# Kernel tuning notes

Hardware: AMD Instinct MI355X
Metric: run time of the kernel (lower is better)

Reference implementation:

```python
import jax, jax.numpy as jnp
import numpy as np

B, P, ENC = 32, 196, 2048   # batch, num_pixels, encoder_dim
A, D, E = 512, 512, 512     # attention_dim, decoder_dim, embed_dim
V, L = 32000, 40            # vocab_size, caption length
T = L - 1                   # max decode steps (static)


def setup_inputs() -> dict:
    key = jax.random.key(0)
    ks = jax.random.split(key, 20)
    u = lambda k, shape, s=0.05: jax.random.uniform(k, shape, jnp.float32, -s, s)
    caplens = jax.random.randint(ks[2], (B,), 5, L + 1).at[0].set(L)
    return {
        "encoder_out": jax.random.normal(ks[0], (B, P, ENC), jnp.float32),
        "encoded_captions": jax.random.randint(ks[1], (B, L), 0, V),
        "caption_lengths": caplens,
        "embedding": u(ks[3], (V, E), 0.1),
        "W_enc": u(ks[4], (ENC, A)), "b_enc": jnp.zeros((A,), jnp.float32),
        "W_dec": u(ks[5], (D, A)),   "b_dec": jnp.zeros((A,), jnp.float32),
        "w_att": u(ks[6], (A, 1)),   "b_att": jnp.zeros((1,), jnp.float32),
        "W_ih": u(ks[7], (E + ENC, 4 * D)), "b_ih": jnp.zeros((4 * D,), jnp.float32),
        "W_hh": u(ks[8], (D, 4 * D)),       "b_hh": jnp.zeros((4 * D,), jnp.float32),
        "W_h": u(ks[9], (ENC, D)),  "b_h": jnp.zeros((D,), jnp.float32),
        "W_c": u(ks[10], (ENC, D)), "b_c": jnp.zeros((D,), jnp.float32),
        "W_fb": u(ks[11], (D, ENC)), "b_fb": jnp.zeros((ENC,), jnp.float32),
        "W_fc": u(ks[12], (D, V), 0.1), "b_fc": jnp.zeros((V,), jnp.float32),
    }


def reference(encoder_out, encoded_captions, caption_lengths, embedding,
              W_enc, b_enc, W_dec, b_dec, w_att, b_att,
              W_ih, b_ih, W_hh, b_hh, W_h, b_h, W_c, b_c,
              W_fb, b_fb, W_fc, b_fc):
    dec_len = caption_lengths - 1                       # [B]
    embs = embedding[encoded_captions]                  # [B, L, E]
    avg = encoder_out.mean(axis=1)                      # [B, ENC]
    h0 = avg @ W_h + b_h                                # [B, D]
    c0 = avg @ W_c + b_c
    enc_att = encoder_out @ W_enc + b_enc               # [B, P, A] (loop-invariant)

    xs = (jnp.transpose(embs[:, :T], (1, 0, 2)), jnp.arange(T))

    def step(carry, xt):
        h, c = carry
        emb_t, t = xt                                   # [B, E], scalar
        active = dec_len > t                            # [B] bool
        dec = h @ W_dec + b_dec                         # [B, A]
        e = (jax.nn.relu(enc_att + dec[:, None, :]) @ w_att)[..., 0] + b_att[0]  # [B, P]
        alpha = jax.nn.softmax(e, axis=1)               # [B, P]
        awe = jnp.einsum('bp,bpd->bd', alpha, encoder_out)
        gate = jax.nn.sigmoid(h @ W_fb + b_fb)          # [B, ENC]
        awe = gate * awe
        x = jnp.concatenate([emb_t, awe], axis=-1)      # [B, E+ENC]
        g = x @ W_ih + b_ih + h @ W_hh + b_hh           # [B, 4D]
        i_, f_, g_, o_ = jnp.split(g, 4, axis=-1)
        c_new = jax.nn.sigmoid(f_) * c + jax.nn.sigmoid(i_) * jnp.tanh(g_)
        h_new = jax.nn.sigmoid(o_) * jnp.tanh(c_new)
        preds = h_new @ W_fc + b_fc                     # [B, V]
        m = active[:, None].astype(h.dtype)
        h = jnp.where(active[:, None], h_new, h)        # only active rows advance
        c = jnp.where(active[:, None], c_new, c)
        return (h, c), (preds * m, alpha * m)

    (_, _), (preds, alphas) = jax.lax.scan(step, (h0, c0), xs)
    predictions = jnp.transpose(preds, (1, 0, 2))       # [B, T, V]
    alphas = jnp.transpose(alphas, (1, 0, 2))           # [B, T, P]
    return predictions, alphas
```

## Files before the change

### kernel.cpp

```cpp
#include <hip/hip_runtime.h>
#include <math.h>

#define NB 32
#define NP 196
#define ENC 2048
#define VOC 32000
#define LCAP 40
#define TS 39

typedef unsigned int uint_t;
typedef unsigned short ushort_t;

__device__ __forceinline__ float sigm(float x) { return 1.f / (1.f + expf(-x)); }

__device__ __forceinline__ ushort_t f2bf(float f) {
  uint_t u = __float_as_uint(f);
  u = (u + 0x7FFFu + ((u >> 16) & 1u)) >> 16;
  return (ushort_t)u;
}
__device__ __forceinline__ float bf2f(ushort_t s) { return __uint_as_float(((uint_t)s) << 16); }

typedef __attribute__((ext_vector_type(8))) short bf8v;
typedef __attribute__((ext_vector_type(16))) float f16v;
typedef __attribute__((ext_vector_type(4))) float f4v;

__device__ __forceinline__ f16v MFMA(bf8v a, bf8v b, f16v c) {
  return __builtin_amdgcn_mfma_f32_32x32x16_bf16(a, b, c, 0, 0, 0);
}

__device__ __forceinline__ void mfma_pipe_frag(
    const ushort_t* __restrict__ pa_h, const ushort_t* __restrict__ pa_l,
    const ushort_t* __restrict__ pb_h, const ushort_t* __restrict__ pb_l,
    int nquad, f16v& acc)
{
  bf8v ah0 = *(const bf8v*)(pa_h +    0), al0 = *(const bf8v*)(pa_l +    0);
  bf8v bh0 = *(const bf8v*)(pb_h +    0), bl0 = *(const bf8v*)(pb_l +    0);
  bf8v ah1 = *(const bf8v*)(pa_h +  512), al1 = *(const bf8v*)(pa_l +  512);
  bf8v bh1 = *(const bf8v*)(pb_h +  512), bl1 = *(const bf8v*)(pb_l +  512);
  bf8v ah2 = *(const bf8v*)(pa_h + 1024), al2 = *(const bf8v*)(pa_l + 1024);
  bf8v bh2 = *(const bf8v*)(pb_h + 1024), bl2 = *(const bf8v*)(pb_l + 1024);
  bf8v ah3 = *(const bf8v*)(pa_h + 1536), al3 = *(const bf8v*)(pa_l + 1536);
  bf8v bh3 = *(const bf8v*)(pb_h + 1536), bl3 = *(const bf8v*)(pb_l + 1536);
  for (int q = 0; q < nquad; ++q) {
    const size_t nk = (size_t)(q + 1) * 2048;
    const bool more = (q + 1 < nquad);
    acc = MFMA(ah0, bh0, acc); acc = MFMA(ah0, bl0, acc); acc = MFMA(al0, bh0, acc);
    if (more) {
      ah0 = *(const bf8v*)(pa_h + nk +    0); al0 = *(const bf8v*)(pa_l + nk +    0);
      bh0 = *(const bf8v*)(pb_h + nk +    0); bl0 = *(const bf8v*)(pb_l + nk +    0);
    }
    acc = MFMA(ah1, bh1, acc); acc = MFMA(ah1, bl1, acc); acc = MFMA(al1, bh1, acc);
    if (more) {
      ah1 = *(const bf8v*)(pa_h + nk +  512); al1 = *(const bf8v*)(pa_l + nk +  512);
      bh1 = *(const bf8v*)(pb_h + nk +  512); bl1 = *(const bf8v*)(pb_l + nk +  512);
    }
    acc = MFMA(ah2, bh2, acc); acc = MFMA(ah2, bl2, acc); acc = MFMA(al2, bh2, acc);
    if (more) {
      ah2 = *(const bf8v*)(pa_h + nk + 1024); al2 = *(const bf8v*)(pa_l + nk + 1024);
      bh2 = *(const bf8v*)(pb_h + nk + 1024); bl2 = *(const bf8v*)(pb_l + nk + 1024);
    }
    acc = MFMA(ah3, bh3, acc); acc = MFMA(ah3, bl3, acc); acc = MFMA(al3, bh3, acc);
    if (more) {
      ah3 = *(const bf8v*)(pa_h + nk + 1536); al3 = *(const bf8v*)(pa_l + nk + 1536);
      bh3 = *(const bf8v*)(pb_h + nk + 1536); bl3 = *(const bf8v*)(pb_l + nk + 1536);
    }
  }
}

__device__ __forceinline__ void mfma_pipe_fragAH(
    const ushort_t* __restrict__ pa_h,
    const ushort_t* __restrict__ pb_h, const ushort_t* __restrict__ pb_l,
    int nquad, f16v& acc)
{
  bf8v ah0 = *(const bf8v*)(pa_h +    0);
  bf8v bh0 = *(const bf8v*)(pb_h +    0), bl0 = *(const bf8v*)(pb_l +    0);
  bf8v ah1 = *(const bf8v*)(pa_h +  512);
  bf8v bh1 = *(const bf8v*)(pb_h +  512), bl1 = *(const bf8v*)(pb_l +  512);
  bf8v ah2 = *(const bf8v*)(pa_h + 1024);
  bf8v bh2 = *(const bf8v*)(pb_h + 1024), bl2 = *(const bf8v*)(pb_l + 1024);
  bf8v ah3 = *(const bf8v*)(pa_h + 1536);
  bf8v bh3 = *(const bf8v*)(pb_h + 1536), bl3 = *(const bf8v*)(pb_l + 1536);
  for (int q = 0; q < nquad; ++q) {
    const size_t nk = (size_t)(q + 1) * 2048;
    const bool more = (q + 1 < nquad);
    acc = MFMA(ah0, bh0, acc); acc = MFMA(ah0, bl0, acc);
    if (more) {
      ah0 = *(const bf8v*)(pa_h + nk +    0);
      bh0 = *(const bf8v*)(pb_h + nk +    0); bl0 = *(const bf8v*)(pb_l + nk +    0);
    }
    acc = MFMA(ah1, bh1, acc); acc = MFMA(ah1, bl1, acc);
    if (more) {
      ah1 = *(const bf8v*)(pa_h + nk +  512);
      bh1 = *(const bf8v*)(pb_h + nk +  512); bl1 = *(const bf8v*)(pb_l + nk +  512);
    }
    acc = MFMA(ah2, bh2, acc); acc = MFMA(ah2, bl2, acc);
    if (more) {
      ah2 = *(const bf8v*)(pa_h + nk + 1024);
      bh2 = *(const bf8v*)(pb_h + nk + 1024); bl2 = *(const bf8v*)(pb_l + nk + 1024);
    }
    acc = MFMA(ah3, bh3, acc); acc = MFMA(ah3, bl3, acc);
    if (more) {
      ah3 = *(const bf8v*)(pa_h + nk + 1536);
      bh3 = *(const bf8v*)(pb_h + nk + 1536); bl3 = *(const bf8v*)(pb_l + nk + 1536);
    }
  }
}

__device__ __forceinline__ void mfma_pipe_fragHH(
    const ushort_t* __restrict__ pa_h,
    const ushort_t* __restrict__ pb_h, int nquad, f16v& acc)
{
  bf8v ah0 = *(const bf8v*)(pa_h +    0);
  bf8v bh0 = *(const bf8v*)(pb_h +    0);
  bf8v ah1 = *(const bf8v*)(pa_h +  512);
  bf8v bh1 = *(const bf8v*)(pb_h +  512);
  bf8v ah2 = *(const bf8v*)(pa_h + 1024);
  bf8v bh2 = *(const bf8v*)(pb_h + 1024);
  bf8v ah3 = *(const bf8v*)(pa_h + 1536);
  bf8v bh3 = *(const bf8v*)(pb_h + 1536);
  for (int q = 0; q < nquad; ++q) {
    const size_t nk = (size_t)(q + 1) * 2048;
    const bool more = (q + 1 < nquad);
    acc = MFMA(ah0, bh0, acc);
    if (more) { ah0 = *(const bf8v*)(pa_h + nk +    0); bh0 = *(const bf8v*)(pb_h + nk +    0); }
    acc = MFMA(ah1, bh1, acc);
    if (more) { ah1 = *(const bf8v*)(pa_h + nk +  512); bh1 = *(const bf8v*)(pb_h + nk +  512); }
    acc = MFMA(ah2, bh2, acc);
    if (more) { ah2 = *(const bf8v*)(pa_h + nk + 1024); bh2 = *(const bf8v*)(pb_h + nk + 1024); }
    acc = MFMA(ah3, bh3, acc);
    if (more) { ah3 = *(const bf8v*)(pa_h + nk + 1536); bh3 = *(const bf8v*)(pb_h + nk + 1536); }
  }
}

#define CD_ROW(rr, g) (((rr) & 3) + 8 * ((rr) >> 2) + 4 * (g))

__global__ __launch_bounds__(256) void menc_att(
    const ushort_t* __restrict__ Ahi,
    const ushort_t* __restrict__ Whi, const ushort_t* __restrict__ Wlo,
    const float* __restrict__ benc, ushort_t* __restrict__ encatt_bf)
{
  __shared__ float tileS[4][32][33];
  int w = threadIdx.x >> 6, lane = threadIdx.x & 63;
  int mt = blockIdx.y;
  int ct = blockIdx.x * 4 + w;
  const ushort_t* pa_h = Ahi + ((size_t)mt * 128) * 512 + lane * 8;
  const ushort_t* pb_h = Whi + ((size_t)ct * 128) * 512 + lane * 8;
  const ushort_t* pb_l = Wlo + ((size_t)ct * 128) * 512 + lane * 8;
  f16v acc = (f16v)(0.0f);
  mfma_pipe_fragAH(pa_h, pb_h, pb_l, 32, acc);
  int r = lane & 31, g = lane >> 5;
  float bn = benc[ct * 32 + r];
#pragma unroll
  for (int rr = 0; rr < 16; ++rr)
    tileS[w][r][CD_ROW(rr, g)] = acc[rr] + bn;
  __syncthreads();
#pragma unroll
  for (int j = 0; j < 4; ++j) {
    int a_l = j * 8 + (lane >> 3);
    int p4 = (lane & 7) * 4;
    int n2 = ct * 32 + a_l;
#pragma unroll
    for (int jj = 0; jj < 4; ++jj) {
      int pl = p4 + jj;
      int rg = mt * 32 + pl;
      int b = rg / 196, pp = rg - b * 196;
      encatt_bf[((size_t)b * 512 + n2) * 196 + pp] = f2bf(tileS[w][a_l][pl]);
    }
  }
}

__global__ __launch_bounds__(256) void mk1(
    const ushort_t* __restrict__ hhi, const ushort_t* __restrict__ hlo,
    const ushort_t* __restrict__ W1hi, const ushort_t* __restrict__ W1lo,
    float* __restrict__ dec_gate)
{
  int w = threadIdx.x >> 6, lane = threadIdx.x & 63;
  int ct = blockIdx.x * 4 + w;
  const ushort_t* pa_h = hhi + lane * 8;
  const ushort_t* pa_l = hlo + lane * 8;
  const ushort_t* pb_h = W1hi + ((size_t)ct * 32) * 512 + lane * 8;
  const ushort_t* pb_l = W1lo + ((size_t)ct * 32) * 512 + lane * 8;
  f16v acc = (f16v)(0.0f);
  mfma_pipe_frag(pa_h, pa_l, pb_h, pb_l, 8, acc);
  int r = lane & 31, g = lane >> 5;
  int n = ct * 32 + r;
#pragma unroll
  for (int rr = 0; rr < 16; ++rr)
    dec_gate[CD_ROW(rr, g) * 2560 + n] = acc[rr];
}

__global__ __launch_bounds__(256) void mk3(
    const ushort_t* __restrict__ xhi, const ushort_t* __restrict__ xlo,
    const ushort_t* __restrict__ W3hi, const ushort_t* __restrict__ W3lo,
    float* __restrict__ P2)
{
  int w = threadIdx.x >> 6, lane = threadIdx.x & 63;
  int ct = blockIdx.x * 4 + w;
  int s = blockIdx.y;
  const ushort_t* pa_h = xhi + ((size_t)s * 20) * 512 + lane * 8;
  const ushort_t* pa_l = xlo + ((size_t)s * 20) * 512 + lane * 8;
  const ushort_t* pb_h = W3hi + ((size_t)ct * 160 + s * 20) * 512 + lane * 8;
  const ushort_t* pb_l = W3lo + ((size_t)ct * 160 + s * 20) * 512 + lane * 8;
  f16v acc = (f16v)(0.0f);
  mfma_pipe_frag(pa_h, pa_l, pb_h, pb_l, 5, acc);
  int r = lane & 31, g = lane >> 5;
  int n = ct * 32 + r;
#pragma unroll
  for (int rr = 0; rr < 16; ++rr)
    P2[(size_t)s * (32 * 2048) + CD_ROW(rr, g) * 2048 + n] = acc[rr];
}

__global__ __launch_bounds__(256) void mpreds(
    const ushort_t* __restrict__ hhist_hi,
    const ushort_t* __restrict__ Wfchi, const float* __restrict__ bfc,
    const int* __restrict__ clen, float* __restrict__ outp)
{
  int orig = blockIdx.x;
  int xcd = orig & 7, i = orig >> 3;
  int base = (xcd < 6) ? xcd * 1219 : 6 * 1219 + (xcd - 6) * 1218;
  int wgid = base + i;
  int ct4 = wgid / 39, mt = wgid - ct4 * 39;
  int w = threadIdx.x >> 6, lane = threadIdx.x & 63;
  int ct = ct4 * 4 + w;
  const ushort_t* pa_h = hhist_hi + ((size_t)mt * 32) * 512 + lane * 8;
  const ushort_t* pb_h = Wfchi + ((size_t)ct * 32) * 512 + lane * 8;
  f16v acc = (f16v)(0.0f);
  mfma_pipe_fragHH(pa_h, pb_h, 8, acc);
  int r = lane & 31, g = lane >> 5;
  int n = ct * 32 + r;
  float bn = bfc[n];
#pragma unroll
  for (int rr = 0; rr < 16; ++rr) {
    int b = CD_ROW(rr, g);
    bool act = clen[b] - 1 > mt;
    outp[(size_t)b * (TS * VOC) + (size_t)mt * VOC + n] = act ? (acc[rr] + bn) : 0.f;
  }
}

__global__ __launch_bounds__(256) void convAe_fused(
    const float* __restrict__ src, ushort_t* __restrict__ dhi,
    ushort_t* __restrict__ enc_bf)
{
  int mt = blockIdx.x;
  int kc = blockIdx.y * 4 + (threadIdx.x >> 6);
  int l = threadIdx.x & 63;
  int r = l & 31, g = l >> 5;
  size_t si = (size_t)(mt * 32 + r) * 2048 + kc * 16 + g * 8;
  const float* s = src + si;
  float4 v0 = *(const float4*)s, v1 = *(const float4*)(s + 4);
  ushort4 h0, h1;
  h0.x = f2bf(v0.x); h0.y = f2bf(v0.y); h0.z = f2bf(v0.z); h0.w = f2bf(v0.w);
  h1.x = f2bf(v1.x); h1.y = f2bf(v1.y); h1.z = f2bf(v1.z); h1.w = f2bf(v1.w);
  size_t off = ((size_t)mt * 128 + kc) * 512 + (size_t)l * 8;
  *(ushort4*)&dhi[off] = h0; *(ushort4*)&dhi[off + 4] = h1;
  *(ushort4*)&enc_bf[si] = h0; *(ushort4*)&enc_bf[si + 4] = h1;
}

__global__ __launch_bounds__(256) void convA_emb_frag(
    const float* __restrict__ Emb, const int* __restrict__ caps,
    ushort_t* __restrict__ dhi, ushort_t* __restrict__ dlo)
{
  int mt = blockIdx.x;
  int kc = blockIdx.y * 4 + (threadIdx.x >> 6);
  int l = threadIdx.x & 63;
  int r = l & 31, g = l >> 5;
  int tok = caps[r * LCAP + mt];
  const float* s = Emb + (size_t)tok * 512 + kc * 16 + g * 8;
  float4 v0 = *(const float4*)s, v1 = *(const float4*)(s + 4);
  ushort4 h0, l0, h1, l1;
  h0.x = f2bf(v0.x); l0.x = f2bf(v0.x - bf2f(h0.x));
  h0.y = f2bf(v0.y); l0.y = f2bf(v0.y - bf2f(h0.y));
  h0.z = f2bf(v0.z); l0.z = f2bf(v0.z - bf2f(h0.z));
  h0.w = f2bf(v0.w); l0.w = f2bf(v0.w - bf2f(h0.w));
  h1.x = f2bf(v1.x); l1.x = f2bf(v1.x - bf2f(h1.x));
  h1.y = f2bf(v1.y); l1.y = f2bf(v1.y - bf2f(h1.y));
  h1.z = f2bf(v1.z); l1.z = f2bf(v1.z - bf2f(h1.z));
  h1.w = f2bf(v1.w); l1.w = f2bf(v1.w - bf2f(h1.w));
  size_t off = ((size_t)mt * 32 + kc) * 512 + (size_t)l * 8;
  *(ushort4*)&dhi[off] = h0; *(ushort4*)&dhi[off + 4] = h1;
  *(ushort4*)&dlo[off] = l0; *(ushort4*)&dlo[off + 4] = l1;
}

__global__ __launch_bounds__(256) void convT_frag(
    const float* __restrict__ src, int N,
    ushort_t* __restrict__ dhi, ushort_t* __restrict__ dlo,
    int nkc_dst, int kc_off)
{
  int ct = blockIdx.x;
  int kc = blockIdx.y * 4 + (threadIdx.x >> 6);
  int l = threadIdx.x & 63;
  int c = l & 31, g = l >> 5;
  const float* s = src + (size_t)(kc * 16 + g * 8) * N + ct * 32 + c;
  ushort_t hi8[8], lo8[8];
#pragma unroll
  for (int e = 0; e < 8; ++e) {
    float f = s[(size_t)e * N];
    hi8[e] = f2bf(f); lo8[e] = f2bf(f - bf2f(hi8[e]));
  }
  size_t off = ((size_t)ct * nkc_dst + kc_off + kc) * 512 + (size_t)l * 8;
  *(ushort4*)&dhi[off]     = make_ushort4(hi8[0], hi8[1], hi8[2], hi8[3]);
  *(ushort4*)&dhi[off + 4] = make_ushort4(hi8[4], hi8[5], hi8[6], hi8[7]);
  *(ushort4*)&dlo[off]     = make_ushort4(lo8[0], lo8[1], lo8[2], lo8[3]);
  *(ushort4*)&dlo[off + 4] = make_ushort4(lo8[4], lo8[5], lo8[6], lo8[7]);
}

__global__ __launch_bounds__(256) void convT_fragH(
    const float* __restrict__ src, int N,
    ushort_t* __restrict__ dhi, int nkc_dst, int kc_off)
{
  int ct = blockIdx.x;
  int kc = blockIdx.y * 4 + (threadIdx.x >> 6);
  int l = threadIdx.x & 63;
  int c = l & 31, g = l >> 5;
  const float* s = src + (size_t)(kc * 16 + g * 8) * N + ct * 32 + c;
  ushort_t hi8[8];
#pragma unroll
  for (int e = 0; e < 8; ++e) hi8[e] = f2bf(s[(size_t)e * N]);
  size_t off = ((size_t)ct * nkc_dst + kc_off + kc) * 512 + (size_t)l * 8;
  *(ushort4*)&dhi[off]     = make_ushort4(hi8[0], hi8[1], hi8[2], hi8[3]);
  *(ushort4*)&dhi[off + 4] = make_ushort4(hi8[4], hi8[5], hi8[6], hi8[7]);
}

__global__ __launch_bounds__(256) void mavg_frag(
    const float* __restrict__ enc, ushort_t* __restrict__ dhi, ushort_t* __restrict__ dlo)
{
  int b = blockIdx.x;
  int e = blockIdx.y * 256 + threadIdx.x;
  float s = 0.f;
  const float* base = enc + (size_t)b * 196 * 2048 + e;
  for (int p = 0; p < NP; ++p) s += base[(size_t)p * 2048];
  s *= (1.f / 196.f);
  ushort_t hi = f2bf(s), lo = f2bf(s - bf2f(hi));
  size_t off = (size_t)(e >> 4) * 512 + ((e >> 3) & 1) * 256 + b * 8 + (e & 7);
  dhi[off] = hi; dlo[off] = lo;
}

__global__ __launch_bounds__(256) void mh0c0(
    const ushort_t* __restrict__ avg_hi, const ushort_t* __restrict__ avg_lo,
    const ushort_t* __restrict__ Whc_hi, const ushort_t* __restrict__ Whc_lo,
    const float* __restrict__ b_h, const float* __restrict__ b_c,
    float* __restrict__ h0f, float* __restrict__ cbuf)
{
  int w = threadIdx.x >> 6, lane = threadIdx.x & 63;
  int ct = blockIdx.x * 4 + w;
  const ushort_t* pa_h = avg_hi + lane * 8;
  const ushort_t* pa_l = avg_lo + lane * 8;
  const ushort_t* pb_h = Whc_hi + ((size_t)ct * 128) * 512 + lane * 8;
  const ushort_t* pb_l = Whc_lo + ((size_t)ct * 128) * 512 + lane * 8;
  f16v acc = (f16v)(0.0f);
  mfma_pipe_frag(pa_h, pa_l, pb_h, pb_l, 32, acc);
  int r = lane & 31, g = lane >> 5;
  int n = ct * 32 + r;
  if (ct < 16) {
    float bn = b_h[n];
#pragma unroll
    for (int rr = 0; rr < 16; ++rr)
      h0f[CD_ROW(rr, g) * 512 + n] = acc[rr] + bn;
  } else {
    int n2 = n - 512;
    float bn = b_c[n2];
#pragma unroll
    for (int rr = 0; rr < 16; ++rr)
      cbuf[CD_ROW(rr, g) * 512 + n2] = acc[rr] + bn;
  }
}

__global__ __launch_bounds__(256) void m_emb(
    const ushort_t* __restrict__ eFhi, const ushort_t* __restrict__ eFlo,
    const ushort_t* __restrict__ Whi, const ushort_t* __restrict__ Wlo,
    const float* __restrict__ b1, const float* __restrict__ b2,
    float* __restrict__ embproj)
{
  int w = threadIdx.x >> 6, lane = threadIdx.x & 63;
  int mt = blockIdx.y;
  int ct = blockIdx.x * 4 + w;
  const ushort_t* pa_h = eFhi + ((size_t)mt * 32) * 512 + lane * 8;
  const ushort_t* pa_l = eFlo + ((size_t)mt * 32) * 512 + lane * 8;
  const ushort_t* pb_h = Whi + ((size_t)ct * 32) * 512 + lane * 8;
  const ushort_t* pb_l = Wlo + ((size_t)ct * 32) * 512 + lane * 8;
  f16v acc = (f16v)(0.0f);
  mfma_pipe_frag(pa_h, pa_l, pb_h, pb_l, 8, acc);
  int r = lane & 31, g = lane >> 5;
  int n = ct * 32 + r;
  float bn = b1[n] + b2[n];
#pragma unroll
  for (int rr = 0; rr < 16; ++rr)
    embproj[(size_t)(mt * 32 + CD_ROW(rr, g)) * 2048 + n] = acc[rr] + bn;
}

__global__ __launch_bounds__(256) void hsplit_frag(
    const float* __restrict__ h0f,
    ushort_t* __restrict__ hhi, ushort_t* __restrict__ hlo,
    ushort_t* __restrict__ xhi, ushort_t* __restrict__ xlo)
{
  int idx = blockIdx.x * 256 + threadIdx.x;
  int b = idx >> 6, dq = idx & 63, d0 = dq << 3;
  ushort4 h0v, h1v, l0v, l1v;
  ushort_t hh[8], hl[8];
#pragma unroll
  for (int j = 0; j < 8; ++j) {
    float v = h0f[b * 512 + d0 + j];
    hh[j] = f2bf(v); hl[j] = f2bf(v - bf2f(hh[j]));
  }
  h0v = make_ushort4(hh[0], hh[1], hh[2], hh[3]); h1v = make_ushort4(hh[4], hh[5], hh[6], hh[7]);
  l0v = make_ushort4(hl[0], hl[1], hl[2], hl[3]); l1v = make_ushort4(hl[4], hl[5], hl[6], hl[7]);
  int kc = d0 >> 4, g = (d0 >> 3) & 1;
  size_t off = ((size_t)kc * 64 + g * 32 + b) * 8;
  *(ushort4*)&hhi[off] = h0v; *(ushort4*)&hhi[off + 4] = h1v;
  *(ushort4*)&hlo[off] = l0v; *(ushort4*)&hlo[off + 4] = l1v;
  int xk0 = 2048 + d0;
  size_t offx = ((size_t)(xk0 >> 4) * 64 + g * 32 + b) * 8;
  *(ushort4*)&xhi[offx] = h0v; *(ushort4*)&xhi[offx + 4] = h1v;
  *(ushort4*)&xlo[offx] = l0v; *(ushort4*)&xlo[offx + 4] = l1v;
}

__global__ __launch_bounds__(512) void k2a_soft(
    const float* __restrict__ dec_gate, const float* __restrict__ bdec,
    const float* __restrict__ watt, const float* __restrict__ batt,
    const ushort_t* __restrict__ encatt_bf, const int* __restrict__ clen,
    float* __restrict__ outa, float* __restrict__ al_ws, int t)
{
  int b = blockIdx.x, tid = threadIdx.x;
  __shared__ float dec_s[512], watt_s[512], part_s[2][256], red_s[256];
  dec_s[tid] = dec_gate[b * 2560 + tid] + bdec[tid];
  watt_s[tid] = watt[tid];
  __syncthreads();
  int p = tid & 255, half = tid >> 8;
  float acc = 0.f;
  if (p < NP) {
    const ushort_t* col = encatt_bf + (size_t)b * 512 * 196 + p;
    int a0 = half * 256;
#pragma unroll 8
    for (int a = a0; a < a0 + 256; ++a)
      acc += fmaxf(bf2f(col[(size_t)a * 196]) + dec_s[a], 0.f) * watt_s[a];
  }
  part_s[half][p] = acc;
  __syncthreads();
  float e = -1e30f;
  if (tid < NP) e = part_s[0][tid] + part_s[1][tid] + batt[0];
  if (tid < 256) red_s[tid] = e;
  __syncthreads();
  for (int wd = 128; wd > 0; wd >>= 1) {
    if (tid < wd) red_s[tid] = fmaxf(red_s[tid], red_s[tid + wd]);
    __syncthreads();
  }
  float m = red_s[0];
  __syncthreads();
  float ex = (tid < NP) ? expf(e - m) : 0.f;
  if (tid < 256) red_s[tid] = ex;
  __syncthreads();
  for (int wd = 128; wd > 0; wd >>= 1) {
    if (tid < wd) red_s[tid] += red_s[tid + wd];
    __syncthreads();
  }
  float inv = 1.f / red_s[0];
  if (tid < NP) {
    float al = ex * inv;
    al_ws[b * NP + tid] = al;
    bool act = clen[b] - 1 > t;
    outa[(size_t)(b * TS + t) * NP + tid] = act ? al : 0.f;
  }
}

__global__ __launch_bounds__(256) void k2b_awe(
    const float* __restrict__ al_ws, const float* __restrict__ dec_gate,
    const float* __restrict__ bfb, const ushort_t* __restrict__ enc_bf,
    ushort_t* __restrict__ xhi, ushort_t* __restrict__ xlo)
{
  int b = blockIdx.x, ds = blockIdx.y, tid = threadIdx.x;
  __shared__ float al_s[196];
  __shared__ float part[8][32][4];
  if (tid < NP) al_s[tid] = al_ws[b * NP + tid];
  __syncthreads();
  int q = tid & 31, sp = tid >> 5;
  int d = ds * 128 + q * 4;
  int p0 = (sp < 4) ? sp * 25 : 100 + (sp - 4) * 24;
  int plen = (sp < 4) ? 25 : 24;
  float ax = 0.f, ay = 0.f, az = 0.f, aw = 0.f;
  for (int p = p0; p < p0 + plen; ++p) {
    float al = al_s[p];
    ushort4 ev = *(const ushort4*)&enc_bf[(size_t)(b * NP + p) * ENC + d];
    ax += al * bf2f(ev.x); ay += al * bf2f(ev.y);
    az += al * bf2f(ev.z); aw += al * bf2f(ev.w);
  }
  part[sp][q][0] = ax; part[sp][q][1] = ay; part[sp][q][2] = az; part[sp][q][3] = aw;
  __syncthreads();
  if (sp == 0) {
    ax = 0.f; ay = 0.f; az = 0.f; aw = 0.f;
#pragma unroll
    for (int s2 = 0; s2 < 8; ++s2) {
      ax += part[s2][q][0]; ay += part[s2][q][1];
      az += part[s2][q][2]; aw += part[s2][q][3];
    }
    float4 gg = *(const float4*)&dec_gate[b * 2560 + 512 + d];
    float4 bb = *(const float4*)&bfb[d];
    float v0 = sigm(gg.x + bb.x) * ax;
    float v1 = sigm(gg.y + bb.y) * ay;
    float v2 = sigm(gg.z + bb.z) * az;
    float v3 = sigm(gg.w + bb.w) * aw;
    ushort4 hi, lo;
    hi.x = f2bf(v0); lo.x = f2bf(v0 - bf2f(hi.x));
    hi.y = f2bf(v1); lo.y = f2bf(v1 - bf2f(hi.y));
    hi.z = f2bf(v2); lo.z = f2bf(v2 - bf2f(hi.z));
    hi.w = f2bf(v3); lo.w = f2bf(v3 - bf2f(hi.w));
    size_t off = ((size_t)(d >> 4) * 64 + ((d >> 3) & 1) * 32 + b) * 8 + (d & 7);
    *(ushort4*)&xhi[off] = hi;
    *(ushort4*)&xlo[off] = lo;
  }
}

__global__ __launch_bounds__(64) void k4_lstm_frag(
    const float* __restrict__ P2, const float* __restrict__ embproj,
    const int* __restrict__ clen, float* __restrict__ c,
    ushort_t* __restrict__ hhi, ushort_t* __restrict__ hlo,
    ushort_t* __restrict__ xhi, ushort_t* __restrict__ xlo,
    ushort_t* __restrict__ hhist_hi, int t)
{
  int idx = blockIdx.x * 64 + threadIdx.x;
  int b = idx >> 6, dq = idx & 63, d0 = dq << 3;
  bool act = clen[b] - 1 > t;
  const float* ep = embproj + (size_t)(t * 32 + b) * 2048;
  f4v i0 = *(const f4v*)&ep[d0],        i1 = *(const f4v*)&ep[d0 + 4];
  f4v f0 = *(const f4v*)&ep[512 + d0],  f1 = *(const f4v*)&ep[512 + d0 + 4];
  f4v g0 = *(const f4v*)&ep[1024 + d0], g1 = *(const f4v*)&ep[1024 + d0 + 4];
  f4v o0 = *(const f4v*)&ep[1536 + d0], o1 = *(const f4v*)&ep[1536 + d0 + 4];
#pragma unroll
  for (int s = 0; s < 8; ++s) {
    const float* p2 = P2 + (size_t)s * 65536 + b * 2048;
    i0 += *(const f4v*)&p2[d0];        i1 += *(const f4v*)&p2[d0 + 4];
    f0 += *(const f4v*)&p2[512 + d0];  f1 += *(const f4v*)&p2[512 + d0 + 4];
    g0 += *(const f4v*)&p2[1024 + d0]; g1 += *(const f4v*)&p2[1024 + d0 + 4];
    o0 += *(const f4v*)&p2[1536 + d0]; o1 += *(const f4v*)&p2[1536 + d0 + 4];
  }
  f4v c0 = *(const f4v*)&c[b * 512 + d0], c1 = *(const f4v*)&c[b * 512 + d0 + 4];
  ushort_t hh[8], hl[8];
  f4v cn0, cn1;
#pragma unroll
  for (int j = 0; j < 8; ++j) {
    float iv = j < 4 ? i0[j] : i1[j - 4];
    float fv = j < 4 ? f0[j] : f1[j - 4];
    float gv = j < 4 ? g0[j] : g1[j - 4];
    float ov = j < 4 ? o0[j] : o1[j - 4];
    float cv = j < 4 ? c0[j] : c1[j - 4];
    float cn = sigm(fv) * cv + sigm(iv) * tanhf(gv);
    float hn = sigm(ov) * tanhf(cn);
    if (j < 4) cn0[j] = cn; else cn1[j - 4] = cn;
    hh[j] = f2bf(hn); hl[j] = f2bf(hn - bf2f(hh[j]));
  }
  ushort4 h0v = make_ushort4(hh[0], hh[1], hh[2], hh[3]);
  ushort4 h1v = make_ushort4(hh[4], hh[5], hh[6], hh[7]);
  ushort4 l0v = make_ushort4(hl[0], hl[1], hl[2], hl[3]);
  ushort4 l1v = make_ushort4(hl[4], hl[5], hl[6], hl[7]);
  int kc = d0 >> 4, g = (d0 >> 3) & 1;
  size_t offh = ((size_t)(t * 32 + kc)) * 512 + ((size_t)g * 32 + b) * 8;
  *(ushort4*)&hhist_hi[offh] = h0v; *(ushort4*)&hhist_hi[offh + 4] = h1v;
  if (!act) return;
  *(f4v*)&c[b * 512 + d0] = cn0; *(f4v*)&c[b * 512 + d0 + 4] = cn1;
  size_t off = ((size_t)kc * 64 + g * 32 + b) * 8;
  *(ushort4*)&hhi[off] = h0v; *(ushort4*)&hhi[off + 4] = h1v;
  *(ushort4*)&hlo[off] = l0v; *(ushort4*)&hlo[off + 4] = l1v;
  int xk0 = 2048 + d0;
  size_t offx = ((size_t)(xk0 >> 4) * 64 + g * 32 + b) * 8;
  *(ushort4*)&xhi[offx] = h0v; *(ushort4*)&xhi[offx + 4] = h1v;
  *(ushort4*)&xlo[offx] = l0v; *(ushort4*)&xlo[offx + 4] = l1v;
}

extern "C" void kernel_launch(void* const* d_in, const int* in_sizes, int n_in,
                              void* d_out, int out_size, void* d_ws, size_t ws_size,
                              hipStream_t stream)
{
  (void)in_sizes; (void)n_in; (void)out_size; (void)ws_size;
  const float* enc   = (const float*)d_in[0];
  const int*   caps  = (const int*)d_in[1];
  const int*   clen  = (const int*)d_in[2];
  const float* emb   = (const float*)d_in[3];
  const float* W_enc = (const float*)d_in[4];
  const float* b_enc = (const float*)d_in[5];
  const float* W_dec = (const float*)d_in[6];
  const float* b_dec = (const float*)d_in[7];
  const float* w_att = (const float*)d_in[8];
  const float* b_att = (const float*)d_in[9];
  const float* W_ih  = (const float*)d_in[10];
  const float* b_ih  = (const float*)d_in[11];
  const float* W_hh  = (const float*)d_in[12];
  const float* b_hh  = (const float*)d_in[13];
  const float* W_h   = (const float*)d_in[14];
  const float* b_h   = (const float*)d_in[15];
  const float* W_c   = (const float*)d_in[16];
  const float* b_c   = (const float*)d_in[17];
  const float* W_fb  = (const float*)d_in[18];
  const float* b_fb  = (const float*)d_in[19];
  const float* W_fc  = (const float*)d_in[20];
  const float* b_fc  = (const float*)d_in[21];

  float* out_preds = (float*)d_out;
  float* out_alpha = out_preds + (size_t)NB * TS * VOC;

  char* p = (char*)d_ws;
  ushort_t* encatt_bf = (ushort_t*)p;     p += 12845056;
  float* embproj  = (float*)p;            p += 10223616;
  float* P2buf    = (float*)p;            p += 2097152;
  float* dec_gate = (float*)p;            p += 327680;
  ushort_t* x_lo  = (ushort_t*)p;         p += 262144;
  float* h0f      = (float*)p;            p += 65536;
  float* cbuf     = (float*)p;            p += 65536;
  float* al_ws    = (float*)p;            p += 25088;
  ushort_t* h_hi  = (ushort_t*)p;         p += 32768;
  ushort_t* h_lo  = (ushort_t*)p;         p += 32768;
  ushort_t* x_hi  = (ushort_t*)p;         p += 163840;
  p += 262144 - 25088 - 32768 - 32768 - 163840;
  ushort_t* e_hi  = (ushort_t*)p;         p += 25690112;
  ushort_t* enc_bf = (ushort_t*)p;        p += 25690112;
  ushort_t* We_hi = (ushort_t*)p;         p += 2097152;
  ushort_t* We_lo = (ushort_t*)p;         p += 2097152;
  ushort_t* W1_hi = (ushort_t*)p;         p += 2621440;
  ushort_t* W1_lo = (ushort_t*)p;         p += 2621440;
  ushort_t* W3_hi = (ushort_t*)p;         p += 10485760;
  ushort_t* W3_lo = (ushort_t*)p;         p += 10485760;
  ushort_t* Wf_hi = (ushort_t*)p;         p += 32768000;
  ushort_t* WiE_hi = (ushort_t*)p;        p += 2097152;
  ushort_t* WiE_lo = (ushort_t*)p;        p += 2097152;
  ushort_t* eF_hi  = (ushort_t*)p;        p += 1277952;
  ushort_t* eF_lo  = (ushort_t*)p;        p += 1277952;
  ushort_t* hh_hi  = (ushort_t*)p;        p += 1277952;

  ushort_t* avg_hi = (ushort_t*)embproj;
  ushort_t* avg_lo = avg_hi + 65536;
  ushort_t* Whc_hi = Wf_hi;
  ushort_t* Whc_lo = Wf_hi + 2097152;

  mavg_frag<<<dim3(32, 8), 256, 0, stream>>>(enc, avg_hi, avg_lo);
  convT_frag<<<dim3(16, 32), 256, 0, stream>>>(W_h, 512, Whc_hi, Whc_lo, 128, 0);
  convT_frag<<<dim3(16, 32), 256, 0, stream>>>(W_c, 512,
      Whc_hi + (size_t)16 * 128 * 512, Whc_lo + (size_t)16 * 128 * 512, 128, 0);
  mh0c0<<<dim3(8), 256, 0, stream>>>(avg_hi, avg_lo, Whc_hi, Whc_lo, b_h, b_c, h0f, cbuf);
  convAe_fused<<<dim3(196, 32), 256, 0, stream>>>(enc, e_hi, enc_bf);
  convT_frag<<<dim3(16, 32), 256, 0, stream>>>(W_enc, 512, We_hi, We_lo, 128, 0);
  convT_frag<<<dim3(16, 8), 256, 0, stream>>>(W_dec, 512, W1_hi, W1_lo, 32, 0);
  convT_frag<<<dim3(64, 8), 256, 0, stream>>>(W_fb, 2048,
      W1_hi + (size_t)16 * 32 * 512, W1_lo + (size_t)16 * 32 * 512, 32, 0);
  convT_frag<<<dim3(64, 32), 256, 0, stream>>>(W_ih + (size_t)512 * 2048, 2048,
      W3_hi, W3_lo, 160, 0);
  convT_frag<<<dim3(64, 8), 256, 0, stream>>>(W_hh, 2048, W3_hi, W3_lo, 160, 128);
  convT_fragH<<<dim3(1000, 8), 256, 0, stream>>>(W_fc, VOC, Wf_hi, 32, 0);
  convA_emb_frag<<<dim3(39, 8), 256, 0, stream>>>(emb, caps, eF_hi, eF_lo);
  convT_frag<<<dim3(64, 8), 256, 0, stream>>>(W_ih, 2048, WiE_hi, WiE_lo, 32, 0);

  menc_att<<<dim3(4, 196), 256, 0, stream>>>(e_hi, We_hi, We_lo, b_enc, encatt_bf);
  m_emb<<<dim3(16, 39), 256, 0, stream>>>(eF_hi, eF_lo, WiE_hi, WiE_lo, b_ih, b_hh, embproj);
  hsplit_frag<<<dim3(8), 256, 0, stream>>>(h0f, h_hi, h_lo, x_hi, x_lo);
  mk1<<<dim3(20), 256, 0, stream>>>(h_hi, h_lo, W1_hi, W1_lo, dec_gate);

  for (int t = 0; t < TS; ++t) {
    k2a_soft<<<dim3(32), 512, 0, stream>>>(dec_gate, b_dec, w_att, b_att,
                                           encatt_bf, clen, out_alpha, al_ws, t);
    k2b_awe<<<dim3(32, 16), 256, 0, stream>>>(al_ws, dec_gate, b_fb, enc_bf, x_hi, x_lo);
    mk3<<<dim3(16, 8), 256, 0, stream>>>(x_hi, x_lo, W3_hi, W3_lo, P2buf);
    k4_lstm_frag<<<dim3(32), 64, 0, stream>>>(P2buf, embproj, clen, cbuf,
                                              h_hi, h_lo, x_hi, x_lo, hh_hi, t);
    if (t < TS - 1)
      mk1<<<dim3(20), 256, 0, stream>>>(h_hi, h_lo, W1_hi, W1_lo, dec_gate);
  }

  mpreds<<<dim3(9750), 256, 0, stream>>>(hh_hi, Wf_hi, b_fc, clen, out_preds);
}
```

Baseline: 2.210 ms.

## Fuse attention softmax and weighted-encoding kernels into one per-step kernel

Merges the per-step softmax kernel and the attention-weighted encoder sum kernel into a single kernel. Each block keeps alpha in shared memory instead of going through a global workspace, and this saves one launch per decode step. The awe reduction is regridded from 32x16 blocks of 256 threads to 32x2 blocks of 512 threads, with the softmax recomputed redundantly in both y-blocks. The cost is far fewer blocks streaming the 25 MB bf16 encoder per step, which may limit memory parallelism.

Result: faster. 2.075 ms (-6.1%).

```diff
diff --git a/kernel.cpp b/kernel.cpp
--- a/kernel.cpp
+++ b/kernel.cpp
@@ -414,14 +414,17 @@
   *(ushort4*)&xlo[offx] = l0v; *(ushort4*)&xlo[offx + 4] = l1v;
 }
 
-__global__ __launch_bounds__(512) void k2a_soft(
+__global__ __launch_bounds__(512) void k2ab(
     const float* __restrict__ dec_gate, const float* __restrict__ bdec,
-    const float* __restrict__ watt, const float* __restrict__ batt,
-    const ushort_t* __restrict__ encatt_bf, const int* __restrict__ clen,
-    float* __restrict__ outa, float* __restrict__ al_ws, int t)
-{
-  int b = blockIdx.x, tid = threadIdx.x;
-  __shared__ float dec_s[512], watt_s[512], part_s[2][256], red_s[256];
+    const float* __restrict__ bfb, const float* __restrict__ watt,
+    const float* __restrict__ batt, const ushort_t* __restrict__ encatt_bf,
+    const ushort_t* __restrict__ enc_bf, const int* __restrict__ clen,
+    float* __restrict__ outa, ushort_t* __restrict__ xhi, ushort_t* __restrict__ xlo,
+    int t)
+{
+  int b = blockIdx.x, yh = blockIdx.y, tid = threadIdx.x;
+  __shared__ float dec_s[512], watt_s[512], part_s[2][256], red_s[256], al_s[196];
+  __shared__ float aw_s[2][256][4];
   dec_s[tid] = dec_gate[b * 2560 + tid] + bdec[tid];
   watt_s[tid] = watt[tid];
   __syncthreads();
@@ -456,42 +459,29 @@
   float inv = 1.f / red_s[0];
   if (tid < NP) {
     float al = ex * inv;
-    al_ws[b * NP + tid] = al;
-    bool act = clen[b] - 1 > t;
-    outa[(size_t)(b * TS + t) * NP + tid] = act ? al : 0.f;
-  }
-}
-
-__global__ __launch_bounds__(256) void k2b_awe(
-    const float* __restrict__ al_ws, const float* __restrict__ dec_gate,
-    const float* __restrict__ bfb, const ushort_t* __restrict__ enc_bf,
-    ushort_t* __restrict__ xhi, ushort_t* __restrict__ xlo)
-{
-  int b = blockIdx.x, ds = blockIdx.y, tid = threadIdx.x;
-  __shared__ float al_s[196];
-  __shared__ float part[8][32][4];
-  if (tid < NP) al_s[tid] = al_ws[b * NP + tid];
-  __syncthreads();
-  int q = tid & 31, sp = tid >> 5;
-  int d = ds * 128 + q * 4;
-  int p0 = (sp < 4) ? sp * 25 : 100 + (sp - 4) * 24;
-  int plen = (sp < 4) ? 25 : 24;
+    al_s[tid] = al;
+    if (yh == 0) {
+      bool act = clen[b] - 1 > t;
+      outa[(size_t)(b * TS + t) * NP + tid] = act ? al : 0.f;
+    }
+  }
+  __syncthreads();
+  int q = tid & 255, sp = tid >> 8;
+  int d = yh * 1024 + q * 4;
   float ax = 0.f, ay = 0.f, az = 0.f, aw = 0.f;
-  for (int p = p0; p < p0 + plen; ++p) {
-    float al = al_s[p];
-    ushort4 ev = *(const ushort4*)&enc_bf[(size_t)(b * NP + p) * ENC + d];
+  int p0 = sp * 98;
+#pragma unroll 7
+  for (int pp = p0; pp < p0 + 98; ++pp) {
+    float al = al_s[pp];
+    ushort4 ev = *(const ushort4*)&enc_bf[(size_t)(b * NP + pp) * ENC + d];
     ax += al * bf2f(ev.x); ay += al * bf2f(ev.y);
     az += al * bf2f(ev.z); aw += al * bf2f(ev.w);
   }
-  part[sp][q][0] = ax; part[sp][q][1] = ay; part[sp][q][2] = az; part[sp][q][3] = aw;
+  aw_s[sp][q][0] = ax; aw_s[sp][q][1] = ay; aw_s[sp][q][2] = az; aw_s[sp][q][3] = aw;
   __syncthreads();
   if (sp == 0) {
-    ax = 0.f; ay = 0.f; az = 0.f; aw = 0.f;
-#pragma unroll
-    for (int s2 = 0; s2 < 8; ++s2) {
-      ax += part[s2][q][0]; ay += part[s2][q][1];
-      az += part[s2][q][2]; aw += part[s2][q][3];
-    }
+    ax += aw_s[1][q][0]; ay += aw_s[1][q][1];
+    az += aw_s[1][q][2]; aw += aw_s[1][q][3];
     float4 gg = *(const float4*)&dec_gate[b * 2560 + 512 + d];
     float4 bb = *(const float4*)&bfb[d];
     float v0 = sigm(gg.x + bb.x) * ax;
@@ -623,6 +613,7 @@
   ushort_t* eF_hi  = (ushort_t*)p;        p += 1277952;
   ushort_t* eF_lo  = (ushort_t*)p;        p += 1277952;
   ushort_t* hh_hi  = (ushort_t*)p;        p += 1277952;
+  (void)al_ws;
 
   ushort_t* avg_hi = (ushort_t*)embproj;
   ushort_t* avg_lo = avg_hi + 65536;
@@ -652,9 +643,9 @@
   mk1<<<dim3(20), 256, 0, stream>>>(h_hi, h_lo, W1_hi, W1_lo, dec_gate);
 
   for (int t = 0; t < TS; ++t) {
-    k2a_soft<<<dim3(32), 512, 0, stream>>>(dec_gate, b_dec, w_att, b_att,
-                                           encatt_bf, clen, out_alpha, al_ws, t);
-    k2b_awe<<<dim3(32, 16), 256, 0, stream>>>(al_ws, dec_gate, b_fb, enc_bf, x_hi, x_lo);
+    k2ab<<<dim3(32, 2), 512, 0, stream>>>(dec_gate, b_dec, b_fb, w_att, b_att,
+                                          encatt_bf, enc_bf, clen, out_alpha,
+                                          x_hi, x_lo, t);
     mk3<<<dim3(16, 8), 256, 0, stream>>>(x_hi, x_lo, W3_hi, W3_lo, P2buf);
     k4_lstm_frag<<<dim3(32), 64, 0, stream>>>(P2buf, embproj, clen, cbuf,
                                               h_hi, h_lo, x_hi, x_lo, hh_hi, t);
```
